# Performance work log

Hardware: AMD Instinct MI355X
Metric: run time of the kernel (lower is better)

The kernel has to match this reference:

```python
import jax, jax.numpy as jnp
import numpy as np

B, S, H, D = 2, 2048, 16, 64
DIM = H * D          # 1024, fused QKV dense outputs 3*DIM
EPS = 1e-6
NINF = -10000.0      # additive mask value from module
STD = 0.02           # truncated-normal init stddev (plain normal here)


def setup_inputs() -> dict:
    key = jax.random.key(0)
    k0, k1, k2 = jax.random.split(key, 3)
    x = jax.random.normal(k0, (B, S, DIM), jnp.float32)
    ln_g = jnp.ones((DIM,), jnp.float32)
    ln_b = jnp.zeros((DIM,), jnp.float32)
    wqkv = jax.random.normal(k1, (DIM, 3 * DIM), jnp.float32) * STD
    bqkv = jnp.zeros((3 * DIM,), jnp.float32)
    wo = jax.random.normal(k2, (DIM, DIM), jnp.float32) * STD
    bo = jnp.zeros((DIM,), jnp.float32)
    return {"x": x, "ln_g": ln_g, "ln_b": ln_b, "wqkv": wqkv,
            "bqkv": bqkv, "wo": wo, "bo": bo}


def reference(x, ln_g, ln_b, wqkv, bqkv, wo, bo):
    b, s, _ = x.shape
    # pre-norm LayerNorm (axis=-1, eps=1e-6)
    mu = jnp.mean(x, axis=-1, keepdims=True)
    var = jnp.mean(jnp.square(x - mu), axis=-1, keepdims=True)
    h = (x - mu) * jax.lax.rsqrt(var + EPS) * ln_g + ln_b
    # fused QKV projection, split along feature axis
    qkv = h @ wqkv + bqkv                       # [b, s, 3*DIM]
    q, k, v = jnp.split(qkv, 3, axis=2)

    def heads(t):                               # [b, s, DIM] -> [b, H, s, D]
        return t.reshape(b, s, H, D).transpose(0, 2, 1, 3)

    q, k, v = heads(q), heads(k), heads(v)
    scores = jnp.einsum("bhqd,bhkd->bhqk", q, k) / jnp.sqrt(jnp.float32(D))
    # causal mask: positions j > i get ninf (mask=None path, Lq == Lk)
    causal = (jnp.arange(s)[:, None] < jnp.arange(s)[None, :]).astype(jnp.float32) * NINF
    a = jax.nn.softmax(scores + causal, axis=-1)  # attdrop rate 0 -> identity
    ctx = jnp.einsum("bhqk,bhkd->bhqd", a, v)
    ctx = ctx.transpose(0, 2, 1, 3).reshape(b, s, DIM)
    # output dense + residual (drop rate 0 -> identity)
    return x + ctx @ wo + bo
```

## Files before the change

kernel.cpp:

```cpp
#include <hip/hip_runtime.h>
#include <hip/hip_bf16.h>

#define B_   2
#define S_   2048
#define H_   16
#define D_   64
#define DIM_ 1024
#define QKV_SZ (32 * 2048 * 64)

typedef __attribute__((ext_vector_type(8))) short bf16x8;
typedef __attribute__((ext_vector_type(4))) float f32x4;
typedef unsigned short u16;
typedef unsigned int u32;

static __device__ __forceinline__ u16 f2bf(float f) {
    union { float f; unsigned u; } v; v.f = f;
    unsigned u = v.u;
    unsigned r = (u + 0x7fffu + ((u >> 16) & 1u)) >> 16;
    return (u16)r;
}
static __device__ __forceinline__ float exp2_fast(float x) {
    float r; asm("v_exp_f32 %0, %1" : "=v"(r) : "v"(x)); return r;
}
static __device__ __forceinline__ u32 cvtpk_bf16(float lo, float hi) {
    u32 r; asm("v_cvt_pk_bf16_f32 %0, %1, %2" : "=v"(r) : "v"(lo), "v"(hi)); return r;
}
static __device__ __forceinline__ void gload_lds16(const u16* g, u16* l) {
    __builtin_amdgcn_global_load_lds(
        (const __attribute__((address_space(1))) void*)g,
        (__attribute__((address_space(3))) void*)l, 16, 0, 0);
}

__global__ __launch_bounds__(256) void prep_kernel(
    const float* __restrict__ x, const float* __restrict__ g,
    const float* __restrict__ b, u16* __restrict__ hb,
    const float* __restrict__ wqkv, u16* __restrict__ wqkvT)
{
    __shared__ u16 T[64][65];
    __shared__ float rs[4], rss[4];
    int bid = blockIdx.x;
    int t = threadIdx.x;
    if (bid < 4096) {
        int row = bid;
        const float4 v = ((const float4*)(x + row * DIM_))[t];
        float s  = v.x + v.y + v.z + v.w;
        float ss = v.x*v.x + v.y*v.y + v.z*v.z + v.w*v.w;
#pragma unroll
        for (int m = 1; m < 64; m <<= 1) { s += __shfl_xor(s, m); ss += __shfl_xor(ss, m); }
        int wid = t >> 6, lane = t & 63;
        if (lane == 0) { rs[wid] = s; rss[wid] = ss; }
        __syncthreads();
        s  = rs[0] + rs[1] + rs[2] + rs[3];
        ss = rss[0] + rss[1] + rss[2] + rss[3];
        float mu   = s * (1.0f / DIM_);
        float var  = ss * (1.0f / DIM_) - mu * mu;
        float rstd = rsqrtf(var + 1e-6f);
        const float4 gv = ((const float4*)g)[t];
        const float4 bv = ((const float4*)b)[t];
        ushort4 ov;
        ov.x = f2bf((v.x - mu) * rstd * gv.x + bv.x);
        ov.y = f2bf((v.y - mu) * rstd * gv.y + bv.y);
        ov.z = f2bf((v.z - mu) * rstd * gv.z + bv.z);
        ov.w = f2bf((v.w - mu) * rstd * gv.w + bv.w);
        ((ushort4*)(hb + row * DIM_))[t] = ov;
    } else {
        int idx = bid - 4096;
        int c0 = (idx % 48) * 64, r0 = (idx / 48) * 64;
        const int R = 1024, C = 3072;
        int rl = t >> 4, cl = (t & 15) * 4;
#pragma unroll
        for (int p = 0; p < 4; p++) {
            float4 v = *(const float4*)(wqkv + (size_t)(r0 + rl + p * 16) * C + c0 + cl);
            T[cl + 0][rl + p * 16] = f2bf(v.x);
            T[cl + 1][rl + p * 16] = f2bf(v.y);
            T[cl + 2][rl + p * 16] = f2bf(v.z);
            T[cl + 3][rl + p * 16] = f2bf(v.w);
        }
        __syncthreads();
#pragma unroll
        for (int p = 0; p < 4; p++) {
            ushort4 o;
            o.x = T[rl + p * 16][cl + 0];
            o.y = T[rl + p * 16][cl + 1];
            o.z = T[rl + p * 16][cl + 2];
            o.w = T[rl + p * 16][cl + 3];
            *(ushort4*)(wqkvT + (size_t)(c0 + rl + p * 16) * R + r0 + cl) = o;
        }
    }
}

__global__ __launch_bounds__(256) void transpose_f32_bf16(
    const float* __restrict__ src, u16* __restrict__ dst, int R, int C)
{
    __shared__ u16 T[64][65];
    int c0 = blockIdx.x * 64, r0 = blockIdx.y * 64;
    int t = threadIdx.x;
    int rl = t >> 4, cl = (t & 15) * 4;
#pragma unroll
    for (int p = 0; p < 4; p++) {
        float4 v = *(const float4*)(src + (size_t)(r0 + rl + p * 16) * C + c0 + cl);
        T[cl + 0][rl + p * 16] = f2bf(v.x);
        T[cl + 1][rl + p * 16] = f2bf(v.y);
        T[cl + 2][rl + p * 16] = f2bf(v.z);
        T[cl + 3][rl + p * 16] = f2bf(v.w);
    }
    __syncthreads();
#pragma unroll
    for (int p = 0; p < 4; p++) {
        ushort4 o;
        o.x = T[rl + p * 16][cl + 0];
        o.y = T[rl + p * 16][cl + 1];
        o.z = T[rl + p * 16][cl + 2];
        o.w = T[rl + p * 16][cl + 3];
        *(ushort4*)(dst + (size_t)(c0 + rl + p * 16) * R + r0 + cl) = o;
    }
}

__global__ __launch_bounds__(256) void qkv_gemm128(
    const u16* __restrict__ A, const u16* __restrict__ Bw,
    const float* __restrict__ bias, u16* __restrict__ qkv)
{
    __shared__ __align__(16) u16 As[2][128 * 32];
    __shared__ __align__(16) u16 Bs[2][128 * 32];
    int t = threadIdx.x;
    int bn = blockIdx.x * 128, bm = blockIdx.y * 128;
    int wid = t >> 6, lane = t & 63;
    int wm = wid >> 1, wn = wid & 1;
    int l15 = lane & 15, l4 = lane >> 4;

    f32x4 zero = {0.f, 0.f, 0.f, 0.f};
    f32x4 acc[4][4];
#pragma unroll
    for (int i = 0; i < 4; i++)
#pragma unroll
        for (int j = 0; j < 4; j++) acc[i][j] = zero;

    const u16* aSrc = A  + (size_t)(bm + wid * 32 + (lane >> 2)) * 1024 + (lane & 3) * 8;
    const u16* bSrc = Bw + (size_t)(bn + wid * 32 + (lane >> 2)) * 1024 + (lane & 3) * 8;

#define STAGE_G(bufsel, kk) do { \
        char* Ad = (char*)As + (bufsel) * 8192 + wid * 2048; \
        char* Bd = (char*)Bs + (bufsel) * 8192 + wid * 2048; \
        gload_lds16(aSrc + (kk),             (u16*)Ad); \
        gload_lds16(aSrc + (kk) + 16 * 1024, (u16*)(Ad + 1024)); \
        gload_lds16(bSrc + (kk),             (u16*)Bd); \
        gload_lds16(bSrc + (kk) + 16 * 1024, (u16*)(Bd + 1024)); \
    } while (0)

    STAGE_G(0, 0);
    __syncthreads();
    int cur = 0;
    for (int kt = 0; kt < 32; ++kt) {
        if (kt < 31) STAGE_G(cur ^ 1, (kt + 1) * 32);
        const char* Ab = (const char*)As + cur * 8192;
        const char* Bb = (const char*)Bs + cur * 8192;
        bf16x8 af[4], bf[4];
#pragma unroll
        for (int mi = 0; mi < 4; mi++)
            af[mi] = *(const bf16x8*)(Ab + (wm * 64 + mi * 16 + l15) * 64 + l4 * 16);
#pragma unroll
        for (int ni = 0; ni < 4; ni++)
            bf[ni] = *(const bf16x8*)(Bb + (wn * 64 + ni * 16 + l15) * 64 + l4 * 16);
        __builtin_amdgcn_s_setprio(1);
#pragma unroll
        for (int mi = 0; mi < 4; mi++)
#pragma unroll
            for (int ni = 0; ni < 4; ni++)
                acc[mi][ni] = __builtin_amdgcn_mfma_f32_16x16x32_bf16(af[mi], bf[ni], acc[mi][ni], 0, 0, 0);
        __builtin_amdgcn_s_setprio(0);
        __syncthreads();
        cur ^= 1;
    }
#pragma unroll
    for (int mi = 0; mi < 4; mi++)
#pragma unroll
        for (int ni = 0; ni < 4; ni++) {
            int col = bn + wn * 64 + ni * 16 + l15;
            int which = col >> 10, f = col & 1023;
            int hh = f >> 6, d = f & 63;
            float bs = bias[col];
            if (which == 2) {
                int s_base = bm + wm * 64 + mi * 16 + l4 * 4;
                int bb = s_base >> 11, s = s_base & 2047;
                ushort4 pk;
                pk.x = f2bf(acc[mi][ni][0] + bs);
                pk.y = f2bf(acc[mi][ni][1] + bs);
                pk.z = f2bf(acc[mi][ni][2] + bs);
                pk.w = f2bf(acc[mi][ni][3] + bs);
                *(ushort4*)(qkv + (size_t)2 * QKV_SZ +
                            ((size_t)(bb * 16 + hh) * 64 + d) * 2048 + s) = pk;
            } else {
                float scl = (which == 0) ? 0.18033688011112042f : 1.0f;
#pragma unroll
                for (int r = 0; r < 4; r++) {
                    int row = bm + wm * 64 + mi * 16 + l4 * 4 + r;
                    int bb = row >> 11, s = row & 2047;
                    qkv[(size_t)which * QKV_SZ + ((size_t)(bb * 16 + hh) * 2048 + s) * 64 + d] =
                        f2bf((acc[mi][ni][r] + bs) * scl);
                }
            }
        }
}

__global__ __launch_bounds__(256) void out_gemm128(
    const u16* __restrict__ A, const u16* __restrict__ Bw,
    const float* __restrict__ bias, const float* __restrict__ xres,
    float* __restrict__ out)
{
    __shared__ __align__(16) u16 As[2][128 * 32];
    __shared__ __align__(16) u16 Bs[2][64 * 32];
    int t = threadIdx.x;
    int bn = blockIdx.x * 64, bm = blockIdx.y * 128;
    int wid = t >> 6, lane = t & 63;
    int l15 = lane & 15, l4 = lane >> 4;

    f32x4 zero = {0.f, 0.f, 0.f, 0.f};
    f32x4 acc[2][4];
#pragma unroll
    for (int i = 0; i < 2; i++)
#pragma unroll
        for (int j = 0; j < 4; j++) acc[i][j] = zero;

    const u16* aSrc = A  + (size_t)(bm + (t >> 2)) * 1024 + (t & 3) * 8;
    const u16* bSrc = Bw + (size_t)(bn + (t >> 2)) * 1024 + (t & 3) * 8;

#define OSTG(bufsel, kk) do { \
        char* Ad = (char*)As + (bufsel) * 8192 + wid * 1024; \
        char* Bd = (char*)Bs + (bufsel) * 4096 + wid * 1024; \
        gload_lds16(aSrc + (kk),             (u16*)Ad); \
        gload_lds16(aSrc + (kk) + 64 * 1024, (u16*)(Ad + 4096)); \
        gload_lds16(bSrc + (kk),             (u16*)Bd); \
    } while (0)

    OSTG(0, 0);
    __syncthreads();
    int cur = 0;
    for (int kt = 0; kt < 32; ++kt) {
        if (kt < 31) OSTG(cur ^ 1, (kt + 1) * 32);
        const char* Ab = (const char*)As + cur * 8192;
        const char* Bb = (const char*)Bs + cur * 4096;
        bf16x8 af[2], bf[4];
#pragma unroll
        for (int mi = 0; mi < 2; mi++)
            af[mi] = *(const bf16x8*)(Ab + (wid * 32 + mi * 16 + l15) * 64 + l4 * 16);
#pragma unroll
        for (int ni = 0; ni < 4; ni++)
            bf[ni] = *(const bf16x8*)(Bb + (ni * 16 + l15) * 64 + l4 * 16);
        __builtin_amdgcn_s_setprio(1);
#pragma unroll
        for (int mi = 0; mi < 2; mi++)
#pragma unroll
            for (int ni = 0; ni < 4; ni++)
                acc[mi][ni] = __builtin_amdgcn_mfma_f32_16x16x32_bf16(af[mi], bf[ni], acc[mi][ni], 0, 0, 0);
        __builtin_amdgcn_s_setprio(0);
        __syncthreads();
        cur ^= 1;
    }
#pragma unroll
    for (int mi = 0; mi < 2; mi++)
#pragma unroll
        for (int ni = 0; ni < 4; ni++) {
            int col = bn + ni * 16 + l15;
            float bs = bias[col];
#pragma unroll
            for (int r = 0; r < 4; r++) {
                int row = bm + wid * 32 + mi * 16 + l4 * 4 + r;
                out[(size_t)row * 1024 + col] = xres[(size_t)row * 1024 + col] + acc[mi][ni][r] + bs;
            }
        }
}

__global__ __launch_bounds__(256) void attn_kernel(
    const u16* __restrict__ qbuf, const u16* __restrict__ kbuf,
    const u16* __restrict__ vbuf, u16* __restrict__ ctx)
{
    __shared__ __align__(16) char Ks[64 * 128];
    __shared__ __align__(16) char Vt[64 * 128];
    __shared__ __align__(16) char Pb[4 * 16 * 128];

    int t = threadIdx.x, wid = t >> 6, lane = t & 63;
    int l15 = lane & 15, l4 = lane >> 4;
    int idx = blockIdx.x;
    int qt = 31 - (idx >> 5);
    int bh = idx & 31;
    int q0 = qt * 64;
    int sr = t >> 3, g = t & 7;
    int bb = bh >> 4, hh = bh & 15;
    f32x4 zero = {0.f, 0.f, 0.f, 0.f};

    const u16* Q = qbuf + (size_t)(bh * 2048 + q0 + wid * 16) * 64;
    bf16x8 aq0 = *(const bf16x8*)(Q + l15 * 64 + 8 * l4);
    bf16x8 aq1 = *(const bf16x8*)(Q + l15 * 64 + 32 + 8 * l4);

    f32x4 o[4];
#pragma unroll
    for (int f = 0; f < 4; f++) o[f] = zero;
    float m_run = -1e30f;
    float l_run = 0.f;

    int kswz = (16 * g) ^ ((sr & 7) << 4);
    char* Pw = Pb + wid * 2048;
    int prow = l15 * 128;
    int pkey = (l15 & 7) << 4;
    int qloc = wid * 16 + l15;

    const u16* Kbase = kbuf + (size_t)bh * 2048 * 64;
    const u16* Vbase = vbuf + (size_t)bh * 64 * 2048;

    bf16x8 ck0 = *(const bf16x8*)(Kbase + (size_t)sr * 64 + g * 8);
    bf16x8 ck1 = *(const bf16x8*)(Kbase + (size_t)(sr + 32) * 64 + g * 8);
    bf16x8 cv0 = *(const bf16x8*)(Vbase + (size_t)sr * 2048 + g * 8);
    bf16x8 cv1 = *(const bf16x8*)(Vbase + (size_t)(sr + 32) * 2048 + g * 8);

    for (int kt = 0; kt <= qt; ++kt) {
        *(bf16x8*)(Ks + sr * 128 + kswz) = ck0;
        *(bf16x8*)(Ks + (sr + 32) * 128 + kswz) = ck1;
        *(bf16x8*)(Vt + sr * 128 + kswz) = cv0;
        *(bf16x8*)(Vt + (sr + 32) * 128 + kswz) = cv1;
        {
            int nkt = (kt < qt) ? kt + 1 : qt;
            const u16* Kn = Kbase + (size_t)nkt * 64 * 64;
            const u16* Vn = Vbase + (size_t)nkt * 64;
            bf16x8 a = *(const bf16x8*)(Kn + (size_t)sr * 64 + g * 8);
            bf16x8 b = *(const bf16x8*)(Kn + (size_t)(sr + 32) * 64 + g * 8);
            bf16x8 c = *(const bf16x8*)(Vn + (size_t)sr * 2048 + g * 8);
            bf16x8 d = *(const bf16x8*)(Vn + (size_t)(sr + 32) * 2048 + g * 8);
            __syncthreads();

            f32x4 sc[4];
            __builtin_amdgcn_s_setprio(1);
#pragma unroll
            for (int nf = 0; nf < 4; ++nf) {
                int krow = nf * 16 + l15;
                int kkey = (krow & 7) << 4;
                bf16x8 kb0 = *(const bf16x8*)(Ks + krow * 128 + ((16 * l4) ^ kkey));
                bf16x8 kb1 = *(const bf16x8*)(Ks + krow * 128 + ((64 + 16 * l4) ^ kkey));
                f32x4 z = zero;
                z = __builtin_amdgcn_mfma_f32_16x16x32_bf16(kb0, aq0, z, 0, 0, 0);
                z = __builtin_amdgcn_mfma_f32_16x16x32_bf16(kb1, aq1, z, 0, 0, 0);
                sc[nf] = z;
            }
            __builtin_amdgcn_s_setprio(0);

            if (kt == qt) {
#pragma unroll
                for (int nf = 0; nf < 4; nf++)
#pragma unroll
                    for (int r = 0; r < 4; r++) {
                        int ka = nf * 16 + 4 * l4 + r;
                        if (ka > qloc) sc[nf][r] = -1e30f;
                    }
            }
            float lmax = sc[0][0];
#pragma unroll
            for (int nf = 0; nf < 4; nf++)
#pragma unroll
                for (int r = 0; r < 4; r++) lmax = fmaxf(lmax, sc[nf][r]);
            if (__any(lmax > m_run + 10.f)) {
                float m0 = lmax;
                m0 = fmaxf(m0, __shfl_xor(m0, 16));
                m0 = fmaxf(m0, __shfl_xor(m0, 32));
                float mn = fmaxf(m_run, m0);
                float al = exp2_fast(m_run - mn);
                l_run *= al;
                m_run = mn;
                float a0 = __shfl(al, 4 * l4 + 0);
                float a1 = __shfl(al, 4 * l4 + 1);
                float a2 = __shfl(al, 4 * l4 + 2);
                float a3 = __shfl(al, 4 * l4 + 3);
#pragma unroll
                for (int f = 0; f < 4; f++) {
                    o[f][0] *= a0; o[f][1] *= a1; o[f][2] *= a2; o[f][3] *= a3;
                }
            }
            float psum = 0.f;
#pragma unroll
            for (int nf = 0; nf < 4; nf++)
#pragma unroll
                for (int r = 0; r < 4; r++) {
                    float pv = exp2_fast(sc[nf][r] - m_run);
                    sc[nf][r] = pv; psum += pv;
                }
            l_run += psum;
#pragma unroll
            for (int nf = 0; nf < 4; nf++) {
                uint2 w;
                w.x = cvtpk_bf16(sc[nf][0], sc[nf][1]);
                w.y = cvtpk_bf16(sc[nf][2], sc[nf][3]);
                *(uint2*)(Pw + prow + ((nf * 32 + l4 * 8) ^ pkey)) = w;
            }
            __builtin_amdgcn_s_setprio(1);
#pragma unroll
            for (int kk = 0; kk < 2; kk++) {
                bf16x8 pa = *(const bf16x8*)(Pw + prow + ((64 * kk + 16 * l4) ^ pkey));
#pragma unroll
                for (int f = 0; f < 4; f++) {
                    int vrow = f * 16 + l15;
                    int vkey = (vrow & 7) << 4;
                    bf16x8 vb = *(const bf16x8*)(Vt + vrow * 128 + ((64 * kk + 16 * l4) ^ vkey));
                    o[f] = __builtin_amdgcn_mfma_f32_16x16x32_bf16(pa, vb, o[f], 0, 0, 0);
                }
            }
            __builtin_amdgcn_s_setprio(0);
            __syncthreads();
            ck0 = a; ck1 = b; cv0 = c; cv1 = d;
        }
    }
    l_run += __shfl_xor(l_run, 16);
    l_run += __shfl_xor(l_run, 32);
#pragma unroll
    for (int r = 0; r < 4; r++) {
        float lr = __shfl(l_run, 4 * l4 + r);
        float inv = 1.f / lr;
        int qa = q0 + wid * 16 + l4 * 4 + r;
        u16* dst = ctx + (size_t)(bb * 2048 + qa) * 1024 + hh * 64;
#pragma unroll
        for (int f = 0; f < 4; f++) dst[f * 16 + l15] = f2bf(o[f][r] * inv);
    }
}

extern "C" void kernel_launch(void* const* d_in, const int* in_sizes, int n_in,
                              void* d_out, int out_size, void* d_ws, size_t ws_size,
                              hipStream_t stream)
{
    const float* x    = (const float*)d_in[0];
    const float* ln_g = (const float*)d_in[1];
    const float* ln_b = (const float*)d_in[2];
    const float* wqkv = (const float*)d_in[3];
    const float* bqkv = (const float*)d_in[4];
    const float* wo   = (const float*)d_in[5];
    const float* bo   = (const float*)d_in[6];
    float* out = (float*)d_out;

    char* ws = (char*)d_ws;
    u16* hbuf  = (u16*)ws;
    u16* qkvb  = (u16*)(ws + 8388608);
    u16* ctxb  = (u16*)(ws + 33554432);
    u16* wqkvT = ctxb;
    u16* woT   = hbuf;

    prep_kernel<<<4864, 256, 0, stream>>>(x, ln_g, ln_b, hbuf, wqkv, wqkvT);
    qkv_gemm128<<<dim3(24, 32), 256, 0, stream>>>(hbuf, wqkvT, bqkv, qkvb);
    transpose_f32_bf16<<<dim3(16, 16), 256, 0, stream>>>(wo, woT, 1024, 1024);
    attn_kernel<<<1024, 256, 0, stream>>>(
        qkvb, qkvb + QKV_SZ, qkvb + 2 * QKV_SZ, ctxb);
    out_gemm128<<<dim3(16, 32), 256, 0, stream>>>(ctxb, woT, bo, x, out);
}
```

Measured before the change: 118.7 us.

## Triple-buffer LDS staging in QKV and output GEMMs with vmcnt-based waits

```diff
diff --git a/kernel.cpp b/kernel.cpp
--- a/kernel.cpp
+++ b/kernel.cpp
@@ -120,8 +120,8 @@
     const u16* __restrict__ A, const u16* __restrict__ Bw,
     const float* __restrict__ bias, u16* __restrict__ qkv)
 {
-    __shared__ __align__(16) u16 As[2][128 * 32];
-    __shared__ __align__(16) u16 Bs[2][128 * 32];
+    __shared__ __align__(16) u16 As[3][128 * 32];
+    __shared__ __align__(16) u16 Bs[3][128 * 32];
     int t = threadIdx.x;
     int bn = blockIdx.x * 128, bm = blockIdx.y * 128;
     int wid = t >> 6, lane = t & 63;
@@ -138,7 +138,7 @@
     const u16* aSrc = A  + (size_t)(bm + wid * 32 + (lane >> 2)) * 1024 + (lane & 3) * 8;
     const u16* bSrc = Bw + (size_t)(bn + wid * 32 + (lane >> 2)) * 1024 + (lane & 3) * 8;
 
-#define STAGE_G(bufsel, kk) do { \
+#define STAGE_Q(bufsel, kk) do { \
         char* Ad = (char*)As + (bufsel) * 8192 + wid * 2048; \
         char* Bd = (char*)Bs + (bufsel) * 8192 + wid * 2048; \
         gload_lds16(aSrc + (kk),             (u16*)Ad); \
@@ -147,11 +147,18 @@
         gload_lds16(bSrc + (kk) + 16 * 1024, (u16*)(Bd + 1024)); \
     } while (0)
 
-    STAGE_G(0, 0);
-    __syncthreads();
+    STAGE_Q(0, 0);
+    STAGE_Q(1, 32);
     int cur = 0;
     for (int kt = 0; kt < 32; ++kt) {
-        if (kt < 31) STAGE_G(cur ^ 1, (kt + 1) * 32);
+        if (kt < 31) asm volatile("s_waitcnt vmcnt(4)" ::: "memory");
+        else         asm volatile("s_waitcnt vmcnt(0)" ::: "memory");
+        __builtin_amdgcn_s_barrier();
+        asm volatile("" ::: "memory");
+        if (kt < 30) {
+            int sb = cur + 2; if (sb >= 3) sb -= 3;
+            STAGE_Q(sb, (kt + 2) * 32);
+        }
         const char* Ab = (const char*)As + cur * 8192;
         const char* Bb = (const char*)Bs + cur * 8192;
         bf16x8 af[4], bf[4];
@@ -168,8 +175,8 @@
             for (int ni = 0; ni < 4; ni++)
                 acc[mi][ni] = __builtin_amdgcn_mfma_f32_16x16x32_bf16(af[mi], bf[ni], acc[mi][ni], 0, 0, 0);
         __builtin_amdgcn_s_setprio(0);
-        __syncthreads();
-        cur ^= 1;
+        asm volatile("" ::: "memory");
+        cur = (cur >= 2) ? 0 : cur + 1;
     }
 #pragma unroll
     for (int mi = 0; mi < 4; mi++)
@@ -207,8 +214,8 @@
     const float* __restrict__ bias, const float* __restrict__ xres,
     float* __restrict__ out)
 {
-    __shared__ __align__(16) u16 As[2][128 * 32];
-    __shared__ __align__(16) u16 Bs[2][64 * 32];
+    __shared__ __align__(16) u16 As[3][128 * 32];
+    __shared__ __align__(16) u16 Bs[3][64 * 32];
     int t = threadIdx.x;
     int bn = blockIdx.x * 64, bm = blockIdx.y * 128;
     int wid = t >> 6, lane = t & 63;
@@ -224,7 +231,7 @@
     const u16* aSrc = A  + (size_t)(bm + (t >> 2)) * 1024 + (t & 3) * 8;
     const u16* bSrc = Bw + (size_t)(bn + (t >> 2)) * 1024 + (t & 3) * 8;
 
-#define OSTG(bufsel, kk) do { \
+#define STAGE_O(bufsel, kk) do { \
         char* Ad = (char*)As + (bufsel) * 8192 + wid * 1024; \
         char* Bd = (char*)Bs + (bufsel) * 4096 + wid * 1024; \
         gload_lds16(aSrc + (kk),             (u16*)Ad); \
@@ -232,11 +239,18 @@
         gload_lds16(bSrc + (kk),             (u16*)Bd); \
     } while (0)
 
-    OSTG(0, 0);
-    __syncthreads();
+    STAGE_O(0, 0);
+    STAGE_O(1, 32);
     int cur = 0;
     for (int kt = 0; kt < 32; ++kt) {
-        if (kt < 31) OSTG(cur ^ 1, (kt + 1) * 32);
+        if (kt < 31) asm volatile("s_waitcnt vmcnt(3)" ::: "memory");
+        else         asm volatile("s_waitcnt vmcnt(0)" ::: "memory");
+        __builtin_amdgcn_s_barrier();
+        asm volatile("" ::: "memory");
+        if (kt < 30) {
+            int sb = cur + 2; if (sb >= 3) sb -= 3;
+            STAGE_O(sb, (kt + 2) * 32);
+        }
         const char* Ab = (const char*)As + cur * 8192;
         const char* Bb = (const char*)Bs + cur * 4096;
         bf16x8 af[2], bf[4];
@@ -253,8 +267,8 @@
             for (int ni = 0; ni < 4; ni++)
                 acc[mi][ni] = __builtin_amdgcn_mfma_f32_16x16x32_bf16(af[mi], bf[ni], acc[mi][ni], 0, 0, 0);
         __builtin_amdgcn_s_setprio(0);
-        __syncthreads();
-        cur ^= 1;
+        asm volatile("" ::: "memory");
+        cur = (cur >= 2) ? 0 : cur + 1;
     }
 #pragma unroll
     for (int mi = 0; mi < 2; mi++)
```

Result: faster. 115.7 us (-2.6%).

## Fold Wo transpose into prep kernel and XOR-swizzle GEMM LDS tiles

Applied to the files above, without the earlier changes.

```diff
diff --git a/kernel.cpp b/kernel.cpp
--- a/kernel.cpp
+++ b/kernel.cpp
@@ -34,7 +34,8 @@
 __global__ __launch_bounds__(256) void prep_kernel(
     const float* __restrict__ x, const float* __restrict__ g,
     const float* __restrict__ b, u16* __restrict__ hb,
-    const float* __restrict__ wqkv, u16* __restrict__ wqkvT)
+    const float* __restrict__ wqkv, u16* __restrict__ wqkvT,
+    const float* __restrict__ wo, u16* __restrict__ woT)
 {
     __shared__ u16 T[64][65];
     __shared__ float rs[4], rss[4];
@@ -64,13 +65,20 @@
         ov.w = f2bf((v.w - mu) * rstd * gv.w + bv.w);
         ((ushort4*)(hb + row * DIM_))[t] = ov;
     } else {
-        int idx = bid - 4096;
-        int c0 = (idx % 48) * 64, r0 = (idx / 48) * 64;
-        const int R = 1024, C = 3072;
+        const float* src; u16* dst; int R, C, c0, r0;
+        if (bid < 4864) {
+            int idx = bid - 4096;
+            src = wqkv; dst = wqkvT; R = 1024; C = 3072;
+            c0 = (idx % 48) * 64; r0 = (idx / 48) * 64;
+        } else {
+            int idx = bid - 4864;
+            src = wo; dst = woT; R = 1024; C = 1024;
+            c0 = (idx % 16) * 64; r0 = (idx / 16) * 64;
+        }
         int rl = t >> 4, cl = (t & 15) * 4;
 #pragma unroll
         for (int p = 0; p < 4; p++) {
-            float4 v = *(const float4*)(wqkv + (size_t)(r0 + rl + p * 16) * C + c0 + cl);
+            float4 v = *(const float4*)(src + (size_t)(r0 + rl + p * 16) * C + c0 + cl);
             T[cl + 0][rl + p * 16] = f2bf(v.x);
             T[cl + 1][rl + p * 16] = f2bf(v.y);
             T[cl + 2][rl + p * 16] = f2bf(v.z);
@@ -84,35 +92,8 @@
             o.y = T[rl + p * 16][cl + 1];
             o.z = T[rl + p * 16][cl + 2];
             o.w = T[rl + p * 16][cl + 3];
-            *(ushort4*)(wqkvT + (size_t)(c0 + rl + p * 16) * R + r0 + cl) = o;
-        }
-    }
-}
-
-__global__ __launch_bounds__(256) void transpose_f32_bf16(
-    const float* __restrict__ src, u16* __restrict__ dst, int R, int C)
-{
-    __shared__ u16 T[64][65];
-    int c0 = blockIdx.x * 64, r0 = blockIdx.y * 64;
-    int t = threadIdx.x;
-    int rl = t >> 4, cl = (t & 15) * 4;
-#pragma unroll
-    for (int p = 0; p < 4; p++) {
-        float4 v = *(const float4*)(src + (size_t)(r0 + rl + p * 16) * C + c0 + cl);
-        T[cl + 0][rl + p * 16] = f2bf(v.x);
-        T[cl + 1][rl + p * 16] = f2bf(v.y);
-        T[cl + 2][rl + p * 16] = f2bf(v.z);
-        T[cl + 3][rl + p * 16] = f2bf(v.w);
-    }
-    __syncthreads();
-#pragma unroll
-    for (int p = 0; p < 4; p++) {
-        ushort4 o;
-        o.x = T[rl + p * 16][cl + 0];
-        o.y = T[rl + p * 16][cl + 1];
-        o.z = T[rl + p * 16][cl + 2];
-        o.w = T[rl + p * 16][cl + 3];
-        *(ushort4*)(dst + (size_t)(c0 + rl + p * 16) * R + r0 + cl) = o;
+            *(ushort4*)(dst + (size_t)(c0 + rl + p * 16) * R + r0 + cl) = o;
+        }
     }
 }
 
@@ -135,8 +116,10 @@
 #pragma unroll
         for (int j = 0; j < 4; j++) acc[i][j] = zero;
 
-    const u16* aSrc = A  + (size_t)(bm + wid * 32 + (lane >> 2)) * 1024 + (lane & 3) * 8;
-    const u16* bSrc = Bw + (size_t)(bn + wid * 32 + (lane >> 2)) * 1024 + (lane & 3) * 8;
+    int scol = ((lane & 3) ^ ((lane >> 3) & 3)) * 8;
+    const u16* aSrc = A  + (size_t)(bm + wid * 32 + (lane >> 2)) * 1024 + scol;
+    const u16* bSrc = Bw + (size_t)(bn + wid * 32 + (lane >> 2)) * 1024 + scol;
+    int rdk = ((l15 >> 1) & 3) << 4;
 
 #define STAGE_G(bufsel, kk) do { \
         char* Ad = (char*)As + (bufsel) * 8192 + wid * 2048; \
@@ -157,10 +140,10 @@
         bf16x8 af[4], bf[4];
 #pragma unroll
         for (int mi = 0; mi < 4; mi++)
-            af[mi] = *(const bf16x8*)(Ab + (wm * 64 + mi * 16 + l15) * 64 + l4 * 16);
+            af[mi] = *(const bf16x8*)(Ab + (wm * 64 + mi * 16 + l15) * 64 + (l4 * 16 ^ rdk));
 #pragma unroll
         for (int ni = 0; ni < 4; ni++)
-            bf[ni] = *(const bf16x8*)(Bb + (wn * 64 + ni * 16 + l15) * 64 + l4 * 16);
+            bf[ni] = *(const bf16x8*)(Bb + (wn * 64 + ni * 16 + l15) * 64 + (l4 * 16 ^ rdk));
         __builtin_amdgcn_s_setprio(1);
 #pragma unroll
         for (int mi = 0; mi < 4; mi++)
@@ -221,8 +204,10 @@
 #pragma unroll
         for (int j = 0; j < 4; j++) acc[i][j] = zero;
 
-    const u16* aSrc = A  + (size_t)(bm + (t >> 2)) * 1024 + (t & 3) * 8;
-    const u16* bSrc = Bw + (size_t)(bn + (t >> 2)) * 1024 + (t & 3) * 8;
+    int scol = ((t & 3) ^ ((t >> 3) & 3)) * 8;
+    const u16* aSrc = A  + (size_t)(bm + (t >> 2)) * 1024 + scol;
+    const u16* bSrc = Bw + (size_t)(bn + (t >> 2)) * 1024 + scol;
+    int rdk = ((l15 >> 1) & 3) << 4;
 
 #define OSTG(bufsel, kk) do { \
         char* Ad = (char*)As + (bufsel) * 8192 + wid * 1024; \
@@ -242,10 +227,10 @@
         bf16x8 af[2], bf[4];
 #pragma unroll
         for (int mi = 0; mi < 2; mi++)
-            af[mi] = *(const bf16x8*)(Ab + (wid * 32 + mi * 16 + l15) * 64 + l4 * 16);
+            af[mi] = *(const bf16x8*)(Ab + (wid * 32 + mi * 16 + l15) * 64 + (l4 * 16 ^ rdk));
 #pragma unroll
         for (int ni = 0; ni < 4; ni++)
-            bf[ni] = *(const bf16x8*)(Bb + (ni * 16 + l15) * 64 + l4 * 16);
+            bf[ni] = *(const bf16x8*)(Bb + (ni * 16 + l15) * 64 + (l4 * 16 ^ rdk));
         __builtin_amdgcn_s_setprio(1);
 #pragma unroll
         for (int mi = 0; mi < 2; mi++)
@@ -437,11 +422,10 @@
     u16* qkvb  = (u16*)(ws + 8388608);
     u16* ctxb  = (u16*)(ws + 33554432);
     u16* wqkvT = ctxb;
-    u16* woT   = hbuf;
-
-    prep_kernel<<<4864, 256, 0, stream>>>(x, ln_g, ln_b, hbuf, wqkv, wqkvT);
+    u16* woT   = (u16*)(ws + 41943040);
+
+    prep_kernel<<<5120, 256, 0, stream>>>(x, ln_g, ln_b, hbuf, wqkv, wqkvT, wo, woT);
     qkv_gemm128<<<dim3(24, 32), 256, 0, stream>>>(hbuf, wqkvT, bqkv, qkvb);
-    transpose_f32_bf16<<<dim3(16, 16), 256, 0, stream>>>(wo, woT, 1024, 1024);
     attn_kernel<<<1024, 256, 0, stream>>>(
         qkvb, qkvb + QKV_SZ, qkvb + 2 * QKV_SZ, ctxb);
     out_gemm128<<<dim3(16, 32), 256, 0, stream>>>(ctxb, woT, bo, x, out);
```

Result: faster. 114.6 us, median of 3 (-3.5%).
